# Optimization experiments

Hardware: AMD Instinct MI355X
Metric: run time of the kernel (lower is better)

## Reference

```python
import jax, jax.numpy as jnp
import numpy as np

B = 65536
LAYERS = [256, 512, 512, 256]


def setup_inputs() -> dict:
    key = jax.random.key(0)
    ks = jax.random.split(key, 10)
    inp = {"data": jax.random.normal(ks[0], (B, LAYERS[0]), dtype=jnp.float32)}
    for i in range(3):
        n_in, n_out = LAYERS[i], LAYERS[i + 1]
        # link weights ~ U[0,1) like random.random(); bias params[0] zeroed in torch code
        inp[f"W{i+1}"] = jax.random.uniform(ks[1 + 3 * i], (n_in, n_out), dtype=jnp.float32)
        inp[f"b{i+1}"] = jnp.zeros((n_out,), dtype=jnp.float32)
        # per-node activation params a = params[1:6], torch.rand init
        inp[f"a{i+1}"] = jax.random.uniform(ks[2 + 3 * i], (n_out, 5), dtype=jnp.float32)
    return inp


def _act(x, a):
    # x: [B, n], a: [n, 5]; a0*tanh(x)*sin(a1*x+a2) + a3*x + a4  (per-node params broadcast over batch)
    return a[:, 0] * jnp.tanh(x) * jnp.sin(a[:, 1] * x + a[:, 2]) + a[:, 3] * x + a[:, 4]


def reference(data, W1, b1, a1, W2, b2, a2, W3, b3, a3):
    h = _act(data @ W1 + b1, a1)
    h = _act(h @ W2 + b2, a2)
    h = _act(h @ W3 + b3, a3)
    return jax.nn.softmax(h, axis=1)
```

## Files before the change

kernel.cpp:

```cpp
#include <hip/hip_runtime.h>

#define BATCH 65536

typedef float f32x4 __attribute__((ext_vector_type(4)));
typedef _Float16 f16x8 __attribute__((ext_vector_type(8)));
typedef _Float16 f16x4 __attribute__((ext_vector_type(4)));

__device__ __forceinline__ void async_ld16(const void* g, void* l) {
  __builtin_amdgcn_global_load_lds(
      (const __attribute__((address_space(1))) void*)g,
      (__attribute__((address_space(3))) void*)l, 16, 0, 0);
}

__device__ __forceinline__ float act_f(float x, float a0, float a1, float a2,
                                       float a3, float a4) {
  float ax = fabsf(x);
  float e = __builtin_amdgcn_exp2f(ax * -2.8853900817779268f);
  float th = (1.0f - e) * __builtin_amdgcn_rcpf(1.0f + e);
  th = copysignf(th, x);
  float arg = fmaf(a1, x, a2);
  float rev = arg * 0.15915494309189535f;
  rev -= floorf(rev);
  float s = __builtin_amdgcn_sinf(rev);
  return fmaf(a3, x, fmaf(a0 * th, s, a4));
}

__global__ __launch_bounds__(256) void splitT_k(const float* __restrict__ W,
                                                _Float16* __restrict__ hi,
                                                _Float16* __restrict__ lo,
                                                int K, int N) {
  const int i = blockIdx.x * 256 + threadIdx.x;
  if (i >= K * N) return;
  const int k = i / N, n = i % N;
  const float w = W[i];
  const _Float16 h = (_Float16)w;
  hi[(size_t)n * K + k] = h;
  lo[(size_t)n * K + k] = (_Float16)(w - (float)h);
}

__global__ __launch_bounds__(256) void prep_params(const float* __restrict__ b,
                                                   const float* __restrict__ a,
                                                   float* __restrict__ Pt,
                                                   int N) {
  const int c = blockIdx.x * 256 + threadIdx.x;
  if (c >= N) return;
  Pt[c] = b[c];
#pragma unroll
  for (int j = 0; j < 5; ++j) Pt[(1 + j) * N + c] = a[c * 5 + j];
}

__device__ __forceinline__ f32x4 mfma3s(f16x8 wh, f16x8 wl, f16x8 xh,
                                        f16x8 xl, f32x4 c) {
  c = __builtin_amdgcn_mfma_f32_16x16x32_f16(wh, xh, c, 0, 0, 0);
  c = __builtin_amdgcn_mfma_f32_16x16x32_f16(wh, xl, c, 0, 0, 0);
  c = __builtin_amdgcn_mfma_f32_16x16x32_f16(wl, xh, c, 0, 0, 0);
  return c;
}

template <int MT, int NT, bool AF32, bool FINAL, int NW>
__global__ __launch_bounds__(256, NW) void gemm_act(
    const float* __restrict__ Af, const _Float16* __restrict__ Ahi,
    const _Float16* __restrict__ Alo, const _Float16* __restrict__ Bhi,
    const _Float16* __restrict__ Blo, const float* __restrict__ Pt,
    _Float16* __restrict__ Chi, _Float16* __restrict__ Clo,
    float* __restrict__ Cout, int K, int N) {
  constexpr int MB_ = 2 * MT * 16;
  constexpr int NB_ = 2 * NT * 16;
  __shared__ __align__(16) _Float16 sA[MB_ * 64];
  __shared__ __align__(16) _Float16 sB[NB_ * 64];

  const int tid = threadIdx.x;
  const int wv = tid >> 6, lane = tid & 63;
  const int wm = wv >> 1, wn = wv & 1;
  const int m16 = lane & 15, quad = lane >> 4;
  const int row0 = blockIdx.x * MB_;
  const int col0 = blockIdx.y * NB_;
  const int rl4 = lane >> 2, sg4 = (lane & 3) ^ ((rl4 >> 1) & 3);
  const int rl8 = lane >> 3, sg8 = (lane & 7) ^ rl8;
  const int fswz = (quad ^ ((m16 >> 1) & 3)) * 8;

  f32x4 acc[MT][NT];
  const f32x4 zero = {0.f, 0.f, 0.f, 0.f};
#pragma unroll
  for (int i = 0; i < MT; ++i)
#pragma unroll
    for (int j = 0; j < NT; ++j) acc[i][j] = zero;

  const int nk = K >> 5;
  for (int kt = 0; kt < nk; ++kt) {
    const int k0 = kt << 5;
    if constexpr (AF32) {
      float* sAf = (float*)sA;
      constexpr int PW = (MB_ / 8) / 4;
#pragma unroll
      for (int t = 0; t < PW; ++t) {
        const int c = wv * PW + t;
        const size_t ga = (size_t)(row0 + c * 8 + rl8) * K + k0 + sg8 * 4;
        async_ld16(Af + ga, (void*)&sAf[c * 256]);
      }
    } else {
      constexpr int PW = (MB_ / 16) / 4;
#pragma unroll
      for (int t = 0; t < PW; ++t) {
        const int c = wv * PW + t;
        const size_t ga = (size_t)(row0 + c * 16 + rl4) * K + k0 + sg4 * 8;
        async_ld16(Ahi + ga, (void*)&sA[c * 512]);
        async_ld16(Alo + ga, (void*)&sA[MB_ * 32 + c * 512]);
      }
    }
    {
      constexpr int PW = (NB_ / 16) / 4;
#pragma unroll
      for (int t = 0; t < PW; ++t) {
        const int c = wv * PW + t;
        const size_t gb = (size_t)(col0 + c * 16 + rl4) * K + k0 + sg4 * 8;
        async_ld16(Bhi + gb, (void*)&sB[c * 512]);
        async_ld16(Blo + gb, (void*)&sB[NB_ * 32 + c * 512]);
      }
    }
    __syncthreads();

    f16x8 ah[MT], al[MT];
#pragma unroll
    for (int tm = 0; tm < MT; ++tm) {
      const int arow = wm * MT * 16 + tm * 16 + m16;
      if constexpr (AF32) {
        const float* sAf = (const float*)sA + arow * 32;
        const int rc7 = m16 & 7;
        const f32x4 x0 = *(const f32x4*)(sAf + ((2 * quad) ^ rc7) * 4);
        const f32x4 x1 = *(const f32x4*)(sAf + ((2 * quad + 1) ^ rc7) * 4);
#pragma unroll
        for (int j = 0; j < 4; ++j) {
          const _Float16 h0 = (_Float16)x0[j];
          ah[tm][j] = h0;
          al[tm][j] = (_Float16)(x0[j] - (float)h0);
          const _Float16 h1 = (_Float16)x1[j];
          ah[tm][4 + j] = h1;
          al[tm][4 + j] = (_Float16)(x1[j] - (float)h1);
        }
      } else {
        const int idx = arow * 32 + fswz;
        ah[tm] = *(const f16x8*)&sA[idx];
        al[tm] = *(const f16x8*)&sA[MB_ * 32 + idx];
      }
    }
#pragma unroll
    for (int tn = 0; tn < NT; ++tn) {
      const int bcol = wn * NT * 16 + tn * 16 + m16;
      const int idx = bcol * 32 + fswz;
      const f16x8 bh = *(const f16x8*)&sB[idx];
      const f16x8 bl = *(const f16x8*)&sB[NB_ * 32 + idx];
#pragma unroll
      for (int tm = 0; tm < MT; ++tm)
        acc[tm][tn] = mfma3s(bh, bl, ah[tm], al[tm], acc[tm][tn]);
    }
    __syncthreads();
  }

  if constexpr (!FINAL) {
#pragma unroll
    for (int tn = 0; tn < NT; ++tn) {
      const int colb = col0 + wn * NT * 16 + tn * 16 + quad * 4;
      f32x4 P[6];
#pragma unroll
      for (int j = 0; j < 6; ++j) P[j] = *(const f32x4*)&Pt[j * N + colb];
#pragma unroll
      for (int tm = 0; tm < MT; ++tm) {
        const int row = row0 + wm * MT * 16 + tm * 16 + m16;
        f16x4 h4, l4;
#pragma unroll
        for (int r = 0; r < 4; ++r) {
          const float y = act_f(acc[tm][tn][r] + P[0][r], P[1][r], P[2][r],
                                P[3][r], P[4][r], P[5][r]);
          const _Float16 h = (_Float16)y;
          h4[r] = h;
          l4[r] = (_Float16)(y - (float)h);
        }
        const size_t o = (size_t)row * N + colb;
        *(f16x4*)&Chi[o] = h4;
        *(f16x4*)&Clo[o] = l4;
      }
    }
  } else {
    const float L2E = 1.4426950408889634f;
    float mx[MT], sm[MT];
#pragma unroll
    for (int tm = 0; tm < MT; ++tm) mx[tm] = -1e30f;
#pragma unroll
    for (int tn = 0; tn < NT; ++tn) {
      const int colb = wn * NT * 16 + tn * 16 + quad * 4;
      f32x4 P[6];
#pragma unroll
      for (int j = 0; j < 6; ++j) P[j] = *(const f32x4*)&Pt[j * N + colb];
#pragma unroll
      for (int tm = 0; tm < MT; ++tm)
#pragma unroll
        for (int r = 0; r < 4; ++r) {
          const float y = act_f(acc[tm][tn][r] + P[0][r], P[1][r], P[2][r],
                                P[3][r], P[4][r], P[5][r]);
          acc[tm][tn][r] = y;
          mx[tm] = fmaxf(mx[tm], y);
        }
    }
#pragma unroll
    for (int tm = 0; tm < MT; ++tm) {
      mx[tm] = fmaxf(mx[tm], __shfl_xor(mx[tm], 16));
      mx[tm] = fmaxf(mx[tm], __shfl_xor(mx[tm], 32));
    }
#pragma unroll
    for (int tm = 0; tm < MT; ++tm) sm[tm] = 0.f;
#pragma unroll
    for (int tn = 0; tn < NT; ++tn)
#pragma unroll
      for (int tm = 0; tm < MT; ++tm)
#pragma unroll
        for (int r = 0; r < 4; ++r) {
          const float e =
              __builtin_amdgcn_exp2f((acc[tm][tn][r] - mx[tm]) * L2E);
          acc[tm][tn][r] = e;
          sm[tm] += e;
        }
#pragma unroll
    for (int tm = 0; tm < MT; ++tm) {
      sm[tm] += __shfl_xor(sm[tm], 16);
      sm[tm] += __shfl_xor(sm[tm], 32);
    }
    float* part = (float*)sA;
    if (quad == 0) {
#pragma unroll
      for (int tm = 0; tm < MT; ++tm) {
        const int rl = wm * MT * 16 + tm * 16 + m16;
        part[(wn * MB_ + rl) * 2 + 0] = mx[tm];
        part[(wn * MB_ + rl) * 2 + 1] = sm[tm];
      }
    }
    __syncthreads();
    float sc[MT];
#pragma unroll
    for (int tm = 0; tm < MT; ++tm) {
      const int rl = wm * MT * 16 + tm * 16 + m16;
      const float mo = part[((1 - wn) * MB_ + rl) * 2 + 0];
      const float so = part[((1 - wn) * MB_ + rl) * 2 + 1];
      const float M = fmaxf(mx[tm], mo);
      const float a = __builtin_amdgcn_exp2f((mx[tm] - M) * L2E);
      const float b = __builtin_amdgcn_exp2f((mo - M) * L2E);
      sc[tm] = a * __builtin_amdgcn_rcpf(fmaf(sm[tm], a, so * b));
    }
#pragma unroll
    for (int tn = 0; tn < NT; ++tn) {
      const int colb = wn * NT * 16 + tn * 16 + quad * 4;
#pragma unroll
      for (int tm = 0; tm < MT; ++tm) {
        const int row = row0 + wm * MT * 16 + tm * 16 + m16;
        f32x4 v = acc[tm][tn];
#pragma unroll
        for (int r = 0; r < 4; ++r) v[r] *= sc[tm];
        *(f32x4*)&Cout[(size_t)row * 256 + colb] = v;
      }
    }
  }
}

extern "C" void kernel_launch(void* const* d_in, const int* in_sizes, int n_in,
                              void* d_out, int out_size, void* d_ws,
                              size_t ws_size, hipStream_t stream) {
  const float* data = (const float*)d_in[0];
  const float* W1 = (const float*)d_in[1];
  const float* b1 = (const float*)d_in[2];
  const float* a1 = (const float*)d_in[3];
  const float* W2 = (const float*)d_in[4];
  const float* b2 = (const float*)d_in[5];
  const float* a2 = (const float*)d_in[6];
  const float* W3 = (const float*)d_in[7];
  const float* b3 = (const float*)d_in[8];
  const float* a3 = (const float*)d_in[9];
  float* out = (float*)d_out;

  char* ws = (char*)d_ws;
  const size_t KB = 1024;
  _Float16* w1hi = (_Float16*)(ws + 0 * KB);
  _Float16* w1lo = (_Float16*)(ws + 256 * KB);
  _Float16* w2hi = (_Float16*)(ws + 512 * KB);
  _Float16* w2lo = (_Float16*)(ws + 1024 * KB);
  _Float16* w3hi = (_Float16*)(ws + 1536 * KB);
  _Float16* w3lo = (_Float16*)(ws + 1792 * KB);
  float* Pt1 = (float*)(ws + 2048 * KB);
  float* Pt2 = (float*)(ws + 2064 * KB);
  float* Pt3 = (float*)(ws + 2080 * KB);
  _Float16* h1hi = (_Float16*)(ws + 2112 * KB);
  _Float16* h1lo = (_Float16*)(ws + 2112 * KB + (size_t)BATCH * 512 * 2);
  _Float16* h2lo = (_Float16*)(ws + 2112 * KB + (size_t)BATCH * 512 * 4);
  _Float16* h2hi = (_Float16*)d_out;

  splitT_k<<<(256 * 512 + 255) / 256, 256, 0, stream>>>(W1, w1hi, w1lo, 256, 512);
  splitT_k<<<(512 * 512 + 255) / 256, 256, 0, stream>>>(W2, w2hi, w2lo, 512, 512);
  splitT_k<<<(512 * 256 + 255) / 256, 256, 0, stream>>>(W3, w3hi, w3lo, 512, 256);
  prep_params<<<2, 256, 0, stream>>>(b1, a1, Pt1, 512);
  prep_params<<<2, 256, 0, stream>>>(b2, a2, Pt2, 512);
  prep_params<<<1, 256, 0, stream>>>(b3, a3, Pt3, 256);

  gemm_act<4, 4, true, false, 4><<<dim3(BATCH / 128, 4), 256, 0, stream>>>(
      data, nullptr, nullptr, w1hi, w1lo, Pt1, h1hi, h1lo, nullptr, 256, 512);
  gemm_act<4, 4, false, false, 4><<<dim3(BATCH / 128, 4), 256, 0, stream>>>(
      nullptr, h1hi, h1lo, w2hi, w2lo, Pt2, h2hi, h2lo, nullptr, 512, 512);
  gemm_act<4, 8, false, true, 2><<<dim3(BATCH / 128, 1), 256, 0, stream>>>(
      nullptr, h2hi, h2lo, w3hi, w3lo, Pt3, nullptr, nullptr, out, 512, 256);
}
```

Measured before the change: 502.4 us.

## Retile GEMMs to 64x256 blocks with LDS-staged coalesced epilogue stores

Changes block tiling from 128x128 (2x2 waves) to 64 rows by 256 columns, with each wave owning 64 columns and all 64 rows. The grid is reordered so column blocks of the same rows are adjacent. The non-final epilogue now stages activated outputs through swizzled LDS, then writes 16-byte f16x8 hi/lo vectors instead of scattered 8-byte stores. The softmax reduction now combines max and sum across four waves through LDS. The goal is fewer weight-tile reloads per row and more coalesced output writes. The cost is more LDS (40 KB), extra barriers, and fewer rows per block, so the A operand is reread by each column block.

```diff
diff --git a/kernel.cpp b/kernel.cpp
--- a/kernel.cpp
+++ b/kernel.cpp
@@ -4,7 +4,6 @@
 
 typedef float f32x4 __attribute__((ext_vector_type(4)));
 typedef _Float16 f16x8 __attribute__((ext_vector_type(8)));
-typedef _Float16 f16x4 __attribute__((ext_vector_type(4)));
 
 __device__ __forceinline__ void async_ld16(const void* g, void* l) {
   __builtin_amdgcn_global_load_lds(
@@ -57,76 +56,66 @@
   return c;
 }
 
-template <int MT, int NT, bool AF32, bool FINAL, int NW>
+template <bool AF32, bool FINAL, int NW>
 __global__ __launch_bounds__(256, NW) void gemm_act(
     const float* __restrict__ Af, const _Float16* __restrict__ Ahi,
     const _Float16* __restrict__ Alo, const _Float16* __restrict__ Bhi,
     const _Float16* __restrict__ Blo, const float* __restrict__ Pt,
     _Float16* __restrict__ Chi, _Float16* __restrict__ Clo,
     float* __restrict__ Cout, int K, int N) {
-  constexpr int MB_ = 2 * MT * 16;
-  constexpr int NB_ = 2 * NT * 16;
-  __shared__ __align__(16) _Float16 sA[MB_ * 64];
-  __shared__ __align__(16) _Float16 sB[NB_ * 64];
+  __shared__ __align__(16) _Float16 smem[20480];
+  _Float16* sA = smem;
+  _Float16* sB = smem + 4096;
 
   const int tid = threadIdx.x;
   const int wv = tid >> 6, lane = tid & 63;
-  const int wm = wv >> 1, wn = wv & 1;
   const int m16 = lane & 15, quad = lane >> 4;
-  const int row0 = blockIdx.x * MB_;
-  const int col0 = blockIdx.y * NB_;
+  const int col0 = blockIdx.x * 256;
+  const int row0 = blockIdx.y * 64;
   const int rl4 = lane >> 2, sg4 = (lane & 3) ^ ((rl4 >> 1) & 3);
   const int rl8 = lane >> 3, sg8 = (lane & 7) ^ rl8;
   const int fswz = (quad ^ ((m16 >> 1) & 3)) * 8;
-
-  f32x4 acc[MT][NT];
+  const int rc7 = m16 & 7;
+
+  f32x4 acc[4][4];
   const f32x4 zero = {0.f, 0.f, 0.f, 0.f};
 #pragma unroll
-  for (int i = 0; i < MT; ++i)
-#pragma unroll
-    for (int j = 0; j < NT; ++j) acc[i][j] = zero;
+  for (int i = 0; i < 4; ++i)
+#pragma unroll
+    for (int j = 0; j < 4; ++j) acc[i][j] = zero;
 
   const int nk = K >> 5;
   for (int kt = 0; kt < nk; ++kt) {
     const int k0 = kt << 5;
     if constexpr (AF32) {
       float* sAf = (float*)sA;
-      constexpr int PW = (MB_ / 8) / 4;
-#pragma unroll
-      for (int t = 0; t < PW; ++t) {
-        const int c = wv * PW + t;
+#pragma unroll
+      for (int t = 0; t < 2; ++t) {
+        const int c = wv * 2 + t;
         const size_t ga = (size_t)(row0 + c * 8 + rl8) * K + k0 + sg8 * 4;
         async_ld16(Af + ga, (void*)&sAf[c * 256]);
       }
     } else {
-      constexpr int PW = (MB_ / 16) / 4;
-#pragma unroll
-      for (int t = 0; t < PW; ++t) {
-        const int c = wv * PW + t;
-        const size_t ga = (size_t)(row0 + c * 16 + rl4) * K + k0 + sg4 * 8;
-        async_ld16(Ahi + ga, (void*)&sA[c * 512]);
-        async_ld16(Alo + ga, (void*)&sA[MB_ * 32 + c * 512]);
-      }
-    }
-    {
-      constexpr int PW = (NB_ / 16) / 4;
-#pragma unroll
-      for (int t = 0; t < PW; ++t) {
-        const int c = wv * PW + t;
-        const size_t gb = (size_t)(col0 + c * 16 + rl4) * K + k0 + sg4 * 8;
-        async_ld16(Bhi + gb, (void*)&sB[c * 512]);
-        async_ld16(Blo + gb, (void*)&sB[NB_ * 32 + c * 512]);
-      }
-    }
-    __syncthreads();
-
-    f16x8 ah[MT], al[MT];
-#pragma unroll
-    for (int tm = 0; tm < MT; ++tm) {
-      const int arow = wm * MT * 16 + tm * 16 + m16;
+      const int c = wv;
+      const size_t ga = (size_t)(row0 + c * 16 + rl4) * K + k0 + sg4 * 8;
+      async_ld16(Ahi + ga, (void*)&sA[c * 512]);
+      async_ld16(Alo + ga, (void*)&sA[2048 + c * 512]);
+    }
+#pragma unroll
+    for (int t = 0; t < 4; ++t) {
+      const int c = wv * 4 + t;
+      const size_t gb = (size_t)(col0 + c * 16 + rl4) * K + k0 + sg4 * 8;
+      async_ld16(Bhi + gb, (void*)&sB[c * 512]);
+      async_ld16(Blo + gb, (void*)&sB[8192 + c * 512]);
+    }
+    __syncthreads();
+
+    f16x8 ah[4], al[4];
+#pragma unroll
+    for (int tm = 0; tm < 4; ++tm) {
+      const int arow = tm * 16 + m16;
       if constexpr (AF32) {
         const float* sAf = (const float*)sA + arow * 32;
-        const int rc7 = m16 & 7;
         const f32x4 x0 = *(const f32x4*)(sAf + ((2 * quad) ^ rc7) * 4);
         const f32x4 x1 = *(const f32x4*)(sAf + ((2 * quad + 1) ^ rc7) * 4);
 #pragma unroll
@@ -141,59 +130,83 @@
       } else {
         const int idx = arow * 32 + fswz;
         ah[tm] = *(const f16x8*)&sA[idx];
-        al[tm] = *(const f16x8*)&sA[MB_ * 32 + idx];
-      }
-    }
-#pragma unroll
-    for (int tn = 0; tn < NT; ++tn) {
-      const int bcol = wn * NT * 16 + tn * 16 + m16;
+        al[tm] = *(const f16x8*)&sA[2048 + idx];
+      }
+    }
+#pragma unroll
+    for (int tn = 0; tn < 4; ++tn) {
+      const int bcol = wv * 64 + tn * 16 + m16;
       const int idx = bcol * 32 + fswz;
       const f16x8 bh = *(const f16x8*)&sB[idx];
-      const f16x8 bl = *(const f16x8*)&sB[NB_ * 32 + idx];
-#pragma unroll
-      for (int tm = 0; tm < MT; ++tm)
+      const f16x8 bl = *(const f16x8*)&sB[8192 + idx];
+#pragma unroll
+      for (int tm = 0; tm < 4; ++tm)
         acc[tm][tn] = mfma3s(bh, bl, ah[tm], al[tm], acc[tm][tn]);
     }
     __syncthreads();
   }
 
   if constexpr (!FINAL) {
-#pragma unroll
-    for (int tn = 0; tn < NT; ++tn) {
-      const int colb = col0 + wn * NT * 16 + tn * 16 + quad * 4;
-      f32x4 P[6];
-#pragma unroll
-      for (int j = 0; j < 6; ++j) P[j] = *(const f32x4*)&Pt[j * N + colb];
-#pragma unroll
-      for (int tm = 0; tm < MT; ++tm) {
-        const int row = row0 + wm * MT * 16 + tm * 16 + m16;
-        f16x4 h4, l4;
+    float* ly = (float*)smem;
+#pragma unroll
+    for (int p = 0; p < 2; ++p) {
+#pragma unroll
+      for (int j = 0; j < 2; ++j) {
+        const int tn = 2 * p + j;
+        const int colb = col0 + wv * 64 + tn * 16 + quad * 4;
+        f32x4 P[6];
+#pragma unroll
+        for (int q = 0; q < 6; ++q) P[q] = *(const f32x4*)&Pt[q * N + colb];
+#pragma unroll
+        for (int tm = 0; tm < 4; ++tm) {
+          const int row = tm * 16 + m16;
+          f32x4 y;
+#pragma unroll
+          for (int r = 0; r < 4; ++r)
+            y[r] = act_f(acc[tm][tn][r] + P[0][r], P[1][r], P[2][r], P[3][r],
+                         P[4][r], P[5][r]);
+          const int g = (wv * 8 + j * 4 + quad) ^ (row & 7);
+          *(f32x4*)&ly[row * 128 + g * 4] = y;
+        }
+      }
+      __syncthreads();
+#pragma unroll
+      for (int i = 0; i < 4; ++i) {
+        const int u = tid + 256 * i;
+        const int row = u >> 4, oct = u & 15;
+        const int g0 = (2 * oct) ^ (row & 7), g1 = (2 * oct + 1) ^ (row & 7);
+        const f32x4 a = *(const f32x4*)&ly[row * 128 + g0 * 4];
+        const f32x4 b = *(const f32x4*)&ly[row * 128 + g1 * 4];
+        f16x8 h8, l8;
 #pragma unroll
         for (int r = 0; r < 4; ++r) {
-          const float y = act_f(acc[tm][tn][r] + P[0][r], P[1][r], P[2][r],
-                                P[3][r], P[4][r], P[5][r]);
-          const _Float16 h = (_Float16)y;
-          h4[r] = h;
-          l4[r] = (_Float16)(y - (float)h);
-        }
-        const size_t o = (size_t)row * N + colb;
-        *(f16x4*)&Chi[o] = h4;
-        *(f16x4*)&Clo[o] = l4;
-      }
+          const _Float16 ha = (_Float16)a[r];
+          h8[r] = ha;
+          l8[r] = (_Float16)(a[r] - (float)ha);
+          const _Float16 hb = (_Float16)b[r];
+          h8[4 + r] = hb;
+          l8[4 + r] = (_Float16)(b[r] - (float)hb);
+        }
+        const int gcol = (oct >> 2) * 64 + p * 32 + (oct & 3) * 8;
+        const size_t o = (size_t)(row0 + row) * N + col0 + gcol;
+        *(f16x8*)&Chi[o] = h8;
+        *(f16x8*)&Clo[o] = l8;
+      }
+      __syncthreads();
     }
   } else {
     const float L2E = 1.4426950408889634f;
-    float mx[MT], sm[MT];
-#pragma unroll
-    for (int tm = 0; tm < MT; ++tm) mx[tm] = -1e30f;
-#pragma unroll
-    for (int tn = 0; tn < NT; ++tn) {
-      const int colb = wn * NT * 16 + tn * 16 + quad * 4;
+    float mx[4], sm[4];
+#pragma unroll
+    for (int tm = 0; tm < 4; ++tm) mx[tm] = -1e30f;
+#pragma unroll
+    for (int tn = 0; tn < 4; ++tn) {
+      const int colb = wv * 64 + tn * 16 + quad * 4;
       f32x4 P[6];
 #pragma unroll
-      for (int j = 0; j < 6; ++j) P[j] = *(const f32x4*)&Pt[j * N + colb];
-#pragma unroll
-      for (int tm = 0; tm < MT; ++tm)
+      for (int q = 0; q < 6; ++q) P[q] = *(const f32x4*)&Pt[q * 256 + colb];
+#pragma unroll
+      for (int tm = 0; tm < 4; ++tm)
 #pragma unroll
         for (int r = 0; r < 4; ++r) {
           const float y = act_f(acc[tm][tn][r] + P[0][r], P[1][r], P[2][r],
@@ -203,16 +216,29 @@
         }
     }
 #pragma unroll
-    for (int tm = 0; tm < MT; ++tm) {
+    for (int tm = 0; tm < 4; ++tm) {
       mx[tm] = fmaxf(mx[tm], __shfl_xor(mx[tm], 16));
       mx[tm] = fmaxf(mx[tm], __shfl_xor(mx[tm], 32));
     }
-#pragma unroll
-    for (int tm = 0; tm < MT; ++tm) sm[tm] = 0.f;
-#pragma unroll
-    for (int tn = 0; tn < NT; ++tn)
-#pragma unroll
-      for (int tm = 0; tm < MT; ++tm)
+    float* part = (float*)smem;
+    if (quad == 0) {
+#pragma unroll
+      for (int tm = 0; tm < 4; ++tm) part[wv * 64 + tm * 16 + m16] = mx[tm];
+    }
+    __syncthreads();
+#pragma unroll
+    for (int tm = 0; tm < 4; ++tm) {
+      const int rl = tm * 16 + m16;
+      float M = part[rl];
+#pragma unroll
+      for (int w = 1; w < 4; ++w) M = fmaxf(M, part[w * 64 + rl]);
+      mx[tm] = M;
+      sm[tm] = 0.f;
+    }
+#pragma unroll
+    for (int tn = 0; tn < 4; ++tn)
+#pragma unroll
+      for (int tm = 0; tm < 4; ++tm)
 #pragma unroll
         for (int r = 0; r < 4; ++r) {
           const float e =
@@ -221,37 +247,32 @@
           sm[tm] += e;
         }
 #pragma unroll
-    for (int tm = 0; tm < MT; ++tm) {
+    for (int tm = 0; tm < 4; ++tm) {
       sm[tm] += __shfl_xor(sm[tm], 16);
       sm[tm] += __shfl_xor(sm[tm], 32);
     }
-    float* part = (float*)sA;
+    __syncthreads();
     if (quad == 0) {
 #pragma unroll
-      for (int tm = 0; tm < MT; ++tm) {
-        const int rl = wm * MT * 16 + tm * 16 + m16;
-        part[(wn * MB_ + rl) * 2 + 0] = mx[tm];
-        part[(wn * MB_ + rl) * 2 + 1] = sm[tm];
-      }
-    }
-    __syncthreads();
-    float sc[MT];
-#pragma unroll
-    for (int tm = 0; tm < MT; ++tm) {
-      const int rl = wm * MT * 16 + tm * 16 + m16;
-      const float mo = part[((1 - wn) * MB_ + rl) * 2 + 0];
-      const float so = part[((1 - wn) * MB_ + rl) * 2 + 1];
-      const float M = fmaxf(mx[tm], mo);
-      const float a = __builtin_amdgcn_exp2f((mx[tm] - M) * L2E);
-      const float b = __builtin_amdgcn_exp2f((mo - M) * L2E);
-      sc[tm] = a * __builtin_amdgcn_rcpf(fmaf(sm[tm], a, so * b));
-    }
-#pragma unroll
-    for (int tn = 0; tn < NT; ++tn) {
-      const int colb = wn * NT * 16 + tn * 16 + quad * 4;
-#pragma unroll
-      for (int tm = 0; tm < MT; ++tm) {
-        const int row = row0 + wm * MT * 16 + tm * 16 + m16;
+      for (int tm = 0; tm < 4; ++tm)
+        part[256 + wv * 64 + tm * 16 + m16] = sm[tm];
+    }
+    __syncthreads();
+    float sc[4];
+#pragma unroll
+    for (int tm = 0; tm < 4; ++tm) {
+      const int rl = tm * 16 + m16;
+      float S = part[256 + rl];
+#pragma unroll
+      for (int w = 1; w < 4; ++w) S += part[256 + w * 64 + rl];
+      sc[tm] = __builtin_amdgcn_rcpf(S);
+    }
+#pragma unroll
+    for (int tn = 0; tn < 4; ++tn) {
+      const int colb = wv * 64 + tn * 16 + quad * 4;
+#pragma unroll
+      for (int tm = 0; tm < 4; ++tm) {
+        const int row = row0 + tm * 16 + m16;
         f32x4 v = acc[tm][tn];
 #pragma unroll
         for (int r = 0; r < 4; ++r) v[r] *= sc[tm];
@@ -299,10 +320,10 @@
   prep_params<<<2, 256, 0, stream>>>(b2, a2, Pt2, 512);
   prep_params<<<1, 256, 0, stream>>>(b3, a3, Pt3, 256);
 
-  gemm_act<4, 4, true, false, 4><<<dim3(BATCH / 128, 4), 256, 0, stream>>>(
+  gemm_act<true, false, 4><<<dim3(2, BATCH / 64), 256, 0, stream>>>(
       data, nullptr, nullptr, w1hi, w1lo, Pt1, h1hi, h1lo, nullptr, 256, 512);
-  gemm_act<4, 4, false, false, 4><<<dim3(BATCH / 128, 4), 256, 0, stream>>>(
+  gemm_act<false, false, 4><<<dim3(2, BATCH / 64), 256, 0, stream>>>(
       nullptr, h1hi, h1lo, w2hi, w2lo, Pt2, h2hi, h2lo, nullptr, 512, 512);
-  gemm_act<4, 8, false, true, 2><<<dim3(BATCH / 128, 1), 256, 0, stream>>>(
+  gemm_act<false, true, 3><<<dim3(1, BATCH / 64), 256, 0, stream>>>(
       nullptr, h2hi, h2lo, w3hi, w3lo, Pt3, nullptr, nullptr, out, 512, 256);
 }
```

Result: faster. 472.6 us (-5.9%).
